# Kernel optimization log

Measured on AMD Instinct MI355X. Metric: run time of the kernel, lower is better.

## Reference

```python
import jax, jax.numpy as jnp
import numpy as np

B, D_IN, D_H, D_OUT, N_EXP = 65536, 512, 512, 128, 16


def setup_inputs() -> dict:
    key = jax.random.key(0)
    ks = jax.random.split(key, 7)
    x = jax.random.normal(ks[0], (B, D_IN), dtype=jnp.float32)
    num = jax.random.randint(ks[1], (B,), 0, N_EXP)
    c = jax.random.randint(ks[2], (N_EXP,), 0, N_EXP)
    W1 = jax.random.normal(ks[3], (D_IN, D_H), dtype=jnp.float32) * 0.05
    b1 = jax.random.normal(ks[4], (D_H,), dtype=jnp.float32) * 0.05
    We = jax.random.normal(ks[5], (N_EXP, D_H, D_OUT), dtype=jnp.float32) * 0.05
    be = jax.random.normal(ks[6], (N_EXP, D_OUT), dtype=jnp.float32) * 0.05
    return {"x": x, "num": num, "c": c, "W1": W1, "b1": b1, "We": We, "be": be}


def reference(x, num, c, W1, b1, We, be):
    # shared trunk: Linear + ReLU
    h = jax.nn.relu(x @ W1 + b1)                      # [B, D_H]
    # per-sample expert id: layers[c[num[i]]]
    e = c[num]                                        # [B] in [0, N_EXP)
    # compute all expert heads (grouped GEMM), then gather routed output
    all_out = jnp.einsum('bh,eho->beo', h, We) + be[None]   # [B, E, D_OUT]
    routed = all_out[jnp.arange(h.shape[0]), e]             # [B, D_OUT]
    return jax.nn.sigmoid(routed)
```

## Files before the change

kernel.cpp:

```cpp
#include <hip/hip_runtime.h>
#include <stdint.h>

#define D_INC 512
#define D_HC  512
#define D_OC  128
#define N_EXPC 16
#define BROWS 65536
#define BM2   64
#define MAXTILES 1040

typedef __bf16 bf16x8 __attribute__((ext_vector_type(8)));
typedef float f32x4 __attribute__((ext_vector_type(4)));
typedef unsigned int u32x4 __attribute__((ext_vector_type(4)));
typedef unsigned short u16x8 __attribute__((ext_vector_type(8)));

__device__ __forceinline__ unsigned short f2bf(float f) {
    __bf16 b = (__bf16)f;
    return __builtin_bit_cast(unsigned short, b);
}

__device__ __forceinline__ f32x4 mfma_bf16(bf16x8 a, bf16x8 b, f32x4 c) {
    return __builtin_amdgcn_mfma_f32_16x16x32_bf16(a, b, c, 0, 0, 0);
}

__device__ __forceinline__ void gl16(const unsigned short* g, unsigned short* l) {
    __builtin_amdgcn_global_load_lds(
        (const __attribute__((address_space(1))) void*)g,
        (__attribute__((address_space(3))) void*)l, 16, 0, 0);
}

__global__ __launch_bounds__(256) void k_transpose_bf16(
    const float* __restrict__ src, unsigned short* __restrict__ dst,
    int R, int C, long sstride, long dstride)
{
    __shared__ unsigned short tile[64][72];
    src += (size_t)blockIdx.z * sstride;
    dst += (size_t)blockIdx.z * dstride;
    int r0 = blockIdx.x * 64, c0 = blockIdx.y * 64;
    int t = threadIdx.x;
    {
        int r = t >> 2, cc = (t & 3) * 16;
        const float4* p = (const float4*)(src + (size_t)(r0 + r) * C + c0 + cc);
        #pragma unroll
        for (int i = 0; i < 4; i++) {
            float4 v = p[i];
            tile[r][cc + i * 4 + 0] = f2bf(v.x);
            tile[r][cc + i * 4 + 1] = f2bf(v.y);
            tile[r][cc + i * 4 + 2] = f2bf(v.z);
            tile[r][cc + i * 4 + 3] = f2bf(v.w);
        }
    }
    __syncthreads();
    {
        int c = t >> 2, rr = (t & 3) * 16;
        unsigned short buf[16];
        #pragma unroll
        for (int i = 0; i < 16; i++) buf[i] = tile[rr + i][c];
        u16x8* q = (u16x8*)(dst + (size_t)(c0 + c) * R + r0 + rr);
        q[0] = *(u16x8*)&buf[0];
        q[1] = *(u16x8*)&buf[8];
    }
}

__global__ __launch_bounds__(256) void k_hist(
    const int* __restrict__ num, const int* __restrict__ c, int* __restrict__ cnt)
{
    __shared__ int lh[N_EXPC];
    int t = threadIdx.x;
    if (t < N_EXPC) lh[t] = 0;
    __syncthreads();
    for (int i = blockIdx.x * 256 + t; i < BROWS; i += gridDim.x * 256)
        atomicAdd(&lh[c[num[i]]], 1);
    __syncthreads();
    if (t < N_EXPC) atomicAdd(&cnt[t], lh[t]);
}

__global__ __launch_bounds__(64) void k_scan(
    const int* __restrict__ cnt, int* __restrict__ base, int* __restrict__ tbl)
{
    __shared__ int sc[N_EXPC];
    int t = threadIdx.x;
    for (int j = t; j < MAXTILES; j += 64) tbl[j * 3 + 2] = 0;
    if (t < N_EXPC) sc[t] = cnt[t];
    __syncthreads();
    if (t < N_EXPC) {
        int run = 0, trun = 0;
        for (int e = 0; e < t; e++) { run += sc[e]; trun += (sc[e] + BM2 - 1) / BM2; }
        base[t] = run;
        int ce = sc[t];
        for (int k = 0, j = trun; k < ce; k += BM2, j++) {
            tbl[j * 3 + 0] = t;
            tbl[j * 3 + 1] = run + k;
            tbl[j * 3 + 2] = (ce - k < BM2) ? (ce - k) : BM2;
        }
    }
}

__global__ __launch_bounds__(256) void k_scatter(
    const int* __restrict__ num, const int* __restrict__ c,
    int* __restrict__ base, int* __restrict__ idx)
{
    __shared__ int lh[N_EXPC], lbase[N_EXPC];
    int t = threadIdx.x;
    if (t < N_EXPC) lh[t] = 0;
    __syncthreads();
    int i = blockIdx.x * 256 + t;
    int e = c[num[i]];
    int lo = atomicAdd(&lh[e], 1);
    __syncthreads();
    if (t < N_EXPC) lbase[t] = atomicAdd(&base[t], lh[t]);
    __syncthreads();
    idx[lbase[e] + lo] = i;
}

__global__ __launch_bounds__(256, 2) void k_gemm1(
    const float* __restrict__ x, const unsigned short* __restrict__ w1t,
    const float* __restrict__ b1, unsigned short* __restrict__ h)
{
    __shared__ unsigned short lsA[2][128 * 32];
    __shared__ unsigned short lsB[2][128 * 32];

    int bid = blockIdx.x;
    int logical = (bid & 7) * 256 + (bid >> 3);
    int rb = logical >> 2, cb = logical & 3;
    long bm = (long)rb * 128;
    int bn = cb * 128;

    int t = threadIdx.x;
    int l = t & 63, wid = t >> 6;
    int wr = (wid >> 1) * 64, wc = (wid & 1) * 64;
    int lr = l & 15, kc = (l >> 4) * 8;
    int srow = t >> 1, sc = (t & 1) * 16;

    const unsigned short* bsrc0 =
        w1t + (size_t)(bn + wid * 32 + (l >> 2)) * D_INC + (l & 3) * 8;
    const unsigned short* bsrc1 = bsrc0 + (size_t)16 * D_INC;
    const float* xrow = x + (bm + srow) * D_INC + sc;

    f32x4 acc[4][4];
    #pragma unroll
    for (int i = 0; i < 4; i++)
        #pragma unroll
        for (int j = 0; j < 4; j++) acc[i][j] = (f32x4){0.f, 0.f, 0.f, 0.f};

    float4 xv0, xv1, xv2, xv3;
    auto loadA = [&](int k0) {
        const float4* xp = (const float4*)(xrow + k0);
        xv0 = xp[0]; xv1 = xp[1]; xv2 = xp[2]; xv3 = xp[3];
    };
    auto writeA = [&](int buf) {
        u16x8 p0, p1;
        p0[0] = f2bf(xv0.x); p0[1] = f2bf(xv0.y); p0[2] = f2bf(xv0.z); p0[3] = f2bf(xv0.w);
        p0[4] = f2bf(xv1.x); p0[5] = f2bf(xv1.y); p0[6] = f2bf(xv1.z); p0[7] = f2bf(xv1.w);
        p1[0] = f2bf(xv2.x); p1[1] = f2bf(xv2.y); p1[2] = f2bf(xv2.z); p1[3] = f2bf(xv2.w);
        p1[4] = f2bf(xv3.x); p1[5] = f2bf(xv3.y); p1[6] = f2bf(xv3.z); p1[7] = f2bf(xv3.w);
        *(u16x8*)&lsA[buf][srow * 32 + sc] = p0;
        *(u16x8*)&lsA[buf][srow * 32 + sc + 8] = p1;
    };
    auto stageB = [&](int buf, int k0) {
        gl16(bsrc0 + k0, &lsB[buf][(wid * 32) * 32]);
        gl16(bsrc1 + k0, &lsB[buf][(wid * 32 + 16) * 32]);
    };

    loadA(0); stageB(0, 0); writeA(0);
    __syncthreads();
    #pragma unroll 2
    for (int ks = 0; ks < 16; ks++) {
        int cur = ks & 1;
        if (ks < 15) {
            loadA((ks + 1) * 32);
            stageB(cur ^ 1, (ks + 1) * 32);
        }
        bf16x8 af[4], bfr[4];
        #pragma unroll
        for (int i = 0; i < 4; i++) {
            af[i]  = __builtin_bit_cast(bf16x8, *(const u32x4*)&lsA[cur][(wr + i * 16 + lr) * 32 + kc]);
            bfr[i] = __builtin_bit_cast(bf16x8, *(const u32x4*)&lsB[cur][(wc + i * 16 + lr) * 32 + kc]);
        }
        #pragma unroll
        for (int i = 0; i < 4; i++)
            #pragma unroll
            for (int j = 0; j < 4; j++)
                acc[i][j] = mfma_bf16(af[i], bfr[j], acc[i][j]);
        if (ks < 15) writeA(cur ^ 1);
        __syncthreads();
    }

    #pragma unroll
    for (int j = 0; j < 4; j++) {
        int col = bn + wc + j * 16 + lr;
        float bv = b1[col];
        #pragma unroll
        for (int i = 0; i < 4; i++) {
            long row = bm + wr + i * 16 + (l >> 4) * 4;
            #pragma unroll
            for (int r = 0; r < 4; r++) {
                float v = fmaxf(acc[i][j][r] + bv, 0.f);
                h[(row + r) * D_HC + col] = f2bf(v);
            }
        }
    }
}

__global__ __launch_bounds__(256, 2) void k_gemm2g(
    const unsigned short* __restrict__ h, const unsigned short* __restrict__ wet,
    const float* __restrict__ be, const int* __restrict__ idx,
    const int* __restrict__ tbl, float* __restrict__ out)
{
    __shared__ unsigned short lsA[2][BM2 * 32];
    __shared__ unsigned short lsB[2][128 * 32];
    __shared__ int rowid[BM2];

    int bj = blockIdx.x;
    int e = tbl[bj * 3 + 0], s = tbl[bj * 3 + 1], n = tbl[bj * 3 + 2];
    if (n == 0) return;

    int t = threadIdx.x;
    int l = t & 63, wid = t >> 6;
    int wr = (wid >> 1) * 32, wc = (wid & 1) * 64;
    int lr = l & 15, kc = (l >> 4) * 8;

    if (t < BM2) rowid[t] = idx[s + (t < n ? t : n - 1)];
    __syncthreads();

    int arow = wid * 16 + (l >> 2);
    const unsigned short* asrc = h + (size_t)rowid[arow] * D_HC + (l & 3) * 8;
    const unsigned short* wbase = wet + (size_t)e * D_OC * D_HC;
    const unsigned short* bsrc0 =
        wbase + (size_t)(wid * 32 + (l >> 2)) * D_HC + (l & 3) * 8;
    const unsigned short* bsrc1 = bsrc0 + (size_t)16 * D_HC;

    f32x4 acc[2][4];
    #pragma unroll
    for (int i = 0; i < 2; i++)
        #pragma unroll
        for (int j = 0; j < 4; j++) acc[i][j] = (f32x4){0.f, 0.f, 0.f, 0.f};

    auto stage = [&](int buf, int k0) {
        gl16(asrc + k0, &lsA[buf][(wid * 16) * 32]);
        gl16(bsrc0 + k0, &lsB[buf][(wid * 32) * 32]);
        gl16(bsrc1 + k0, &lsB[buf][(wid * 32 + 16) * 32]);
    };

    stage(0, 0);
    __syncthreads();
    #pragma unroll 2
    for (int ks = 0; ks < 16; ks++) {
        int cur = ks & 1;
        if (ks < 15) stage(cur ^ 1, (ks + 1) * 32);
        bf16x8 af[2], bfr[4];
        #pragma unroll
        for (int i = 0; i < 2; i++)
            af[i]  = __builtin_bit_cast(bf16x8, *(const u32x4*)&lsA[cur][(wr + i * 16 + lr) * 32 + kc]);
        #pragma unroll
        for (int j = 0; j < 4; j++)
            bfr[j] = __builtin_bit_cast(bf16x8, *(const u32x4*)&lsB[cur][(wc + j * 16 + lr) * 32 + kc]);
        #pragma unroll
        for (int i = 0; i < 2; i++)
            #pragma unroll
            for (int j = 0; j < 4; j++)
                acc[i][j] = mfma_bf16(af[i], bfr[j], acc[i][j]);
        __syncthreads();
    }

    #pragma unroll
    for (int j = 0; j < 4; j++) {
        int col = wc + j * 16 + lr;
        float bev = be[e * D_OC + col];
        #pragma unroll
        for (int i = 0; i < 2; i++) {
            int rl = wr + i * 16 + (l >> 4) * 4;
            #pragma unroll
            for (int r = 0; r < 4; r++) {
                if (rl + r < n) {
                    float v = acc[i][j][r] + bev;
                    out[(size_t)rowid[rl + r] * D_OC + col] = 1.f / (1.f + __expf(-v));
                }
            }
        }
    }
}

extern "C" void kernel_launch(void* const* d_in, const int* in_sizes, int n_in,
                              void* d_out, int out_size, void* d_ws, size_t ws_size,
                              hipStream_t stream)
{
    const float* x  = (const float*)d_in[0];
    const int* num  = (const int*)d_in[1];
    const int* c    = (const int*)d_in[2];
    const float* W1 = (const float*)d_in[3];
    const float* b1 = (const float*)d_in[4];
    const float* We = (const float*)d_in[5];
    const float* be = (const float*)d_in[6];
    float* out = (float*)d_out;

    uint8_t* p = (uint8_t*)d_ws;
    unsigned short* w1t  = (unsigned short*)p;  p += (size_t)512 * 512 * 2;
    unsigned short* wet  = (unsigned short*)p;  p += (size_t)16 * 128 * 512 * 2;
    unsigned short* hbuf = (unsigned short*)p;  p += (size_t)BROWS * 512 * 2;
    int* cnt  = (int*)p;  p += N_EXPC * 4;
    int* base = (int*)p;  p += N_EXPC * 4;
    int* tbl  = (int*)p;  p += MAXTILES * 3 * 4;
    int* idx  = (int*)p;  p += (size_t)BROWS * 4;

    dim3 b256(256);
    hipMemsetAsync(cnt, 0, N_EXPC * sizeof(int), stream);
    k_hist<<<dim3(256), b256, 0, stream>>>(num, c, cnt);
    k_scan<<<dim3(1), dim3(64), 0, stream>>>(cnt, base, tbl);
    k_scatter<<<dim3(256), b256, 0, stream>>>(num, c, base, idx);
    k_transpose_bf16<<<dim3(8, 8, 1), b256, 0, stream>>>(W1, w1t, 512, 512, 0, 0);
    k_transpose_bf16<<<dim3(8, 2, 16), b256, 0, stream>>>(We, wet, 512, 128,
                                                          (long)512 * 128, (long)512 * 128);
    k_gemm1<<<dim3(2048), b256, 0, stream>>>(x, w1t, b1, hbuf);
    k_gemm2g<<<dim3(MAXTILES), b256, 0, stream>>>(hbuf, wet, be, idx, tbl, out);
}
```

Baseline: 329.3 us.

## Pre-convert x to bf16 and triple-buffer both GEMMs with swizzled LDS

Adds a separate kernel that converts x to bf16 in workspace, so gemm1 can stage both operands with direct global-to-LDS loads instead of register loads plus conversion. Both GEMMs move from double to triple buffering, with manual vmcnt waits and a single barrier per k-step, and use an XOR-swizzled LDS layout to cut bank conflicts. gemm2 also remaps block ids to interleave tiles. In exchange it adds an extra read and write pass over x, keeps a fallback kernel for when the workspace is too small, and increases LDS use, which may lower occupancy.

After: 338.0 us. +2.6%, slower.

```diff
diff --git a/kernel.cpp b/kernel.cpp
--- a/kernel.cpp
+++ b/kernel.cpp
@@ -60,6 +60,18 @@
         q[0] = *(u16x8*)&buf[0];
         q[1] = *(u16x8*)&buf[8];
     }
+}
+
+__global__ __launch_bounds__(256) void k_xconv(
+    const float* __restrict__ x, unsigned short* __restrict__ xb)
+{
+    size_t gid = (size_t)blockIdx.x * 256 + threadIdx.x;
+    const float4* p = (const float4*)x + gid * 2;
+    float4 a = p[0], b = p[1];
+    u16x8 o;
+    o[0] = f2bf(a.x); o[1] = f2bf(a.y); o[2] = f2bf(a.z); o[3] = f2bf(a.w);
+    o[4] = f2bf(b.x); o[5] = f2bf(b.y); o[6] = f2bf(b.z); o[7] = f2bf(b.w);
+    *((u16x8*)xb + gid) = o;
 }
 
 __global__ __launch_bounds__(256) void k_hist(
@@ -114,11 +126,11 @@
 }
 
 __global__ __launch_bounds__(256, 2) void k_gemm1(
-    const float* __restrict__ x, const unsigned short* __restrict__ w1t,
+    const unsigned short* __restrict__ xb, const unsigned short* __restrict__ w1t,
     const float* __restrict__ b1, unsigned short* __restrict__ h)
 {
-    __shared__ unsigned short lsA[2][128 * 32];
-    __shared__ unsigned short lsB[2][128 * 32];
+    __shared__ unsigned short lsA[3][128 * 32];
+    __shared__ unsigned short lsB[3][128 * 32];
 
     int bid = blockIdx.x;
     int logical = (bid & 7) * 256 + (bid >> 3);
@@ -126,23 +138,93 @@
     long bm = (long)rb * 128;
     int bn = cb * 128;
 
-    int t = threadIdx.x;
-    int l = t & 63, wid = t >> 6;
+    int t = threadIdx.x, l = t & 63, wid = t >> 6;
+    int wr = (wid >> 1) * 64, wc = (wid & 1) * 64;
+    int lr = l & 15;
+    int sgr = (((l & 3) ^ ((l >> 3) & 3))) * 8;
+    int sw8 = (((l >> 4) ^ ((l >> 1) & 3))) * 8;
+
+    const unsigned short* asrc0 = xb + (size_t)(bm + wid * 32 + (l >> 2)) * D_INC + sgr;
+    const unsigned short* asrc1 = asrc0 + (size_t)16 * D_INC;
+    const unsigned short* bsrc0 = w1t + (size_t)(bn + wid * 32 + (l >> 2)) * D_INC + sgr;
+    const unsigned short* bsrc1 = bsrc0 + (size_t)16 * D_INC;
+
+    f32x4 acc[4][4];
+    #pragma unroll
+    for (int i = 0; i < 4; i++)
+        #pragma unroll
+        for (int j = 0; j < 4; j++) acc[i][j] = (f32x4){0.f, 0.f, 0.f, 0.f};
+
+    auto stage = [&](int buf, int k0) {
+        gl16(asrc0 + k0, &lsA[buf][(wid * 32) * 32]);
+        gl16(asrc1 + k0, &lsA[buf][(wid * 32 + 16) * 32]);
+        gl16(bsrc0 + k0, &lsB[buf][(wid * 32) * 32]);
+        gl16(bsrc1 + k0, &lsB[buf][(wid * 32 + 16) * 32]);
+    };
+
+    stage(0, 0);
+    stage(1, 32);
+    #pragma unroll
+    for (int ks = 0; ks < 16; ks++) {
+        if (ks < 15) asm volatile("s_waitcnt vmcnt(4)" ::: "memory");
+        else         asm volatile("s_waitcnt vmcnt(0)" ::: "memory");
+        __builtin_amdgcn_s_barrier();
+        __builtin_amdgcn_sched_barrier(0);
+        if (ks + 2 < 16) stage((ks + 2) % 3, (ks + 2) * 32);
+        __builtin_amdgcn_sched_barrier(0);
+        int cur = ks % 3;
+        bf16x8 af[4], bfr[4];
+        #pragma unroll
+        for (int i = 0; i < 4; i++) {
+            af[i]  = __builtin_bit_cast(bf16x8, *(const u32x4*)&lsA[cur][(wr + i * 16 + lr) * 32 + sw8]);
+            bfr[i] = __builtin_bit_cast(bf16x8, *(const u32x4*)&lsB[cur][(wc + i * 16 + lr) * 32 + sw8]);
+        }
+        #pragma unroll
+        for (int i = 0; i < 4; i++)
+            #pragma unroll
+            for (int j = 0; j < 4; j++)
+                acc[i][j] = mfma_bf16(af[i], bfr[j], acc[i][j]);
+    }
+
+    #pragma unroll
+    for (int j = 0; j < 4; j++) {
+        int col = bn + wc + j * 16 + lr;
+        float bv = b1[col];
+        #pragma unroll
+        for (int i = 0; i < 4; i++) {
+            long row = bm + wr + i * 16 + (l >> 4) * 4;
+            #pragma unroll
+            for (int r = 0; r < 4; r++) {
+                float v = fmaxf(acc[i][j][r] + bv, 0.f);
+                h[(row + r) * D_HC + col] = f2bf(v);
+            }
+        }
+    }
+}
+
+__global__ __launch_bounds__(256, 2) void k_gemm1_fb(
+    const float* __restrict__ x, const unsigned short* __restrict__ w1t,
+    const float* __restrict__ b1, unsigned short* __restrict__ h)
+{
+    __shared__ unsigned short lsA[2][128 * 32];
+    __shared__ unsigned short lsB[2][128 * 32];
+    int bid = blockIdx.x;
+    int logical = (bid & 7) * 256 + (bid >> 3);
+    int rb = logical >> 2, cb = logical & 3;
+    long bm = (long)rb * 128;
+    int bn = cb * 128;
+    int t = threadIdx.x, l = t & 63, wid = t >> 6;
     int wr = (wid >> 1) * 64, wc = (wid & 1) * 64;
     int lr = l & 15, kc = (l >> 4) * 8;
     int srow = t >> 1, sc = (t & 1) * 16;
-
-    const unsigned short* bsrc0 =
-        w1t + (size_t)(bn + wid * 32 + (l >> 2)) * D_INC + (l & 3) * 8;
+    const unsigned short* bsrc0 = w1t + (size_t)(bn + wid * 32 + (l >> 2)) * D_INC + (l & 3) * 8;
     const unsigned short* bsrc1 = bsrc0 + (size_t)16 * D_INC;
     const float* xrow = x + (bm + srow) * D_INC + sc;
-
     f32x4 acc[4][4];
     #pragma unroll
     for (int i = 0; i < 4; i++)
         #pragma unroll
         for (int j = 0; j < 4; j++) acc[i][j] = (f32x4){0.f, 0.f, 0.f, 0.f};
-
     float4 xv0, xv1, xv2, xv3;
     auto loadA = [&](int k0) {
         const float4* xp = (const float4*)(xrow + k0);
@@ -161,16 +243,12 @@
         gl16(bsrc0 + k0, &lsB[buf][(wid * 32) * 32]);
         gl16(bsrc1 + k0, &lsB[buf][(wid * 32 + 16) * 32]);
     };
-
     loadA(0); stageB(0, 0); writeA(0);
     __syncthreads();
     #pragma unroll 2
     for (int ks = 0; ks < 16; ks++) {
         int cur = ks & 1;
-        if (ks < 15) {
-            loadA((ks + 1) * 32);
-            stageB(cur ^ 1, (ks + 1) * 32);
-        }
+        if (ks < 15) { loadA((ks + 1) * 32); stageB(cur ^ 1, (ks + 1) * 32); }
         bf16x8 af[4], bfr[4];
         #pragma unroll
         for (int i = 0; i < 4; i++) {
@@ -185,7 +263,6 @@
         if (ks < 15) writeA(cur ^ 1);
         __syncthreads();
     }
-
     #pragma unroll
     for (int j = 0; j < 4; j++) {
         int col = bn + wc + j * 16 + lr;
@@ -207,27 +284,28 @@
     const float* __restrict__ be, const int* __restrict__ idx,
     const int* __restrict__ tbl, float* __restrict__ out)
 {
-    __shared__ unsigned short lsA[2][BM2 * 32];
-    __shared__ unsigned short lsB[2][128 * 32];
+    __shared__ unsigned short lsA[3][BM2 * 32];
+    __shared__ unsigned short lsB[3][128 * 32];
     __shared__ int rowid[BM2];
 
-    int bj = blockIdx.x;
+    int bid = blockIdx.x;
+    int bj = (bid & 7) * 130 + (bid >> 3);
     int e = tbl[bj * 3 + 0], s = tbl[bj * 3 + 1], n = tbl[bj * 3 + 2];
     if (n == 0) return;
 
-    int t = threadIdx.x;
-    int l = t & 63, wid = t >> 6;
+    int t = threadIdx.x, l = t & 63, wid = t >> 6;
     int wr = (wid >> 1) * 32, wc = (wid & 1) * 64;
-    int lr = l & 15, kc = (l >> 4) * 8;
+    int lr = l & 15;
+    int sgr = (((l & 3) ^ ((l >> 3) & 3))) * 8;
+    int sw8 = (((l >> 4) ^ ((l >> 1) & 3))) * 8;
 
     if (t < BM2) rowid[t] = idx[s + (t < n ? t : n - 1)];
     __syncthreads();
 
-    int arow = wid * 16 + (l >> 2);
-    const unsigned short* asrc = h + (size_t)rowid[arow] * D_HC + (l & 3) * 8;
+    const unsigned short* asrc =
+        h + (size_t)rowid[wid * 16 + (l >> 2)] * D_HC + sgr;
     const unsigned short* wbase = wet + (size_t)e * D_OC * D_HC;
-    const unsigned short* bsrc0 =
-        wbase + (size_t)(wid * 32 + (l >> 2)) * D_HC + (l & 3) * 8;
+    const unsigned short* bsrc0 = wbase + (size_t)(wid * 32 + (l >> 2)) * D_HC + sgr;
     const unsigned short* bsrc1 = bsrc0 + (size_t)16 * D_HC;
 
     f32x4 acc[2][4];
@@ -243,24 +321,28 @@
     };
 
     stage(0, 0);
-    __syncthreads();
-    #pragma unroll 2
+    stage(1, 32);
+    #pragma unroll
     for (int ks = 0; ks < 16; ks++) {
-        int cur = ks & 1;
-        if (ks < 15) stage(cur ^ 1, (ks + 1) * 32);
+        if (ks < 15) asm volatile("s_waitcnt vmcnt(3)" ::: "memory");
+        else         asm volatile("s_waitcnt vmcnt(0)" ::: "memory");
+        __builtin_amdgcn_s_barrier();
+        __builtin_amdgcn_sched_barrier(0);
+        if (ks + 2 < 16) stage((ks + 2) % 3, (ks + 2) * 32);
+        __builtin_amdgcn_sched_barrier(0);
+        int cur = ks % 3;
         bf16x8 af[2], bfr[4];
         #pragma unroll
         for (int i = 0; i < 2; i++)
-            af[i]  = __builtin_bit_cast(bf16x8, *(const u32x4*)&lsA[cur][(wr + i * 16 + lr) * 32 + kc]);
+            af[i]  = __builtin_bit_cast(bf16x8, *(const u32x4*)&lsA[cur][(wr + i * 16 + lr) * 32 + sw8]);
         #pragma unroll
         for (int j = 0; j < 4; j++)
-            bfr[j] = __builtin_bit_cast(bf16x8, *(const u32x4*)&lsB[cur][(wc + j * 16 + lr) * 32 + kc]);
+            bfr[j] = __builtin_bit_cast(bf16x8, *(const u32x4*)&lsB[cur][(wc + j * 16 + lr) * 32 + sw8]);
         #pragma unroll
         for (int i = 0; i < 2; i++)
             #pragma unroll
             for (int j = 0; j < 4; j++)
                 acc[i][j] = mfma_bf16(af[i], bfr[j], acc[i][j]);
-        __syncthreads();
     }
 
     #pragma unroll
@@ -294,14 +376,17 @@
     const float* be = (const float*)d_in[6];
     float* out = (float*)d_out;
 
-    uint8_t* p = (uint8_t*)d_ws;
+    uint8_t* p0 = (uint8_t*)d_ws;
+    uint8_t* p = p0;
     unsigned short* w1t  = (unsigned short*)p;  p += (size_t)512 * 512 * 2;
     unsigned short* wet  = (unsigned short*)p;  p += (size_t)16 * 128 * 512 * 2;
     unsigned short* hbuf = (unsigned short*)p;  p += (size_t)BROWS * 512 * 2;
-    int* cnt  = (int*)p;  p += N_EXPC * 4;
-    int* base = (int*)p;  p += N_EXPC * 4;
+    int* cnt  = (int*)p;  p += 64;
+    int* base = (int*)p;  p += 64;
     int* tbl  = (int*)p;  p += MAXTILES * 3 * 4;
     int* idx  = (int*)p;  p += (size_t)BROWS * 4;
+    unsigned short* xbuf = (unsigned short*)p;  p += (size_t)BROWS * 512 * 2;
+    bool big = ((size_t)(p - p0) <= ws_size);
 
     dim3 b256(256);
     hipMemsetAsync(cnt, 0, N_EXPC * sizeof(int), stream);
@@ -311,6 +396,11 @@
     k_transpose_bf16<<<dim3(8, 8, 1), b256, 0, stream>>>(W1, w1t, 512, 512, 0, 0);
     k_transpose_bf16<<<dim3(8, 2, 16), b256, 0, stream>>>(We, wet, 512, 128,
                                                           (long)512 * 128, (long)512 * 128);
-    k_gemm1<<<dim3(2048), b256, 0, stream>>>(x, w1t, b1, hbuf);
+    if (big) {
+        k_xconv<<<dim3(16384), b256, 0, stream>>>(x, xbuf);
+        k_gemm1<<<dim3(2048), b256, 0, stream>>>(xbuf, w1t, b1, hbuf);
+    } else {
+        k_gemm1_fb<<<dim3(2048), b256, 0, stream>>>(x, w1t, b1, hbuf);
+    }
     k_gemm2g<<<dim3(MAXTILES), b256, 0, stream>>>(hbuf, wet, be, idx, tbl, out);
 }
```
